# Optimization experiments

Hardware: AMD Instinct MI355X
Metric: run time of the kernel (lower is better)

Reference implementation:

```python
import jax, jax.numpy as jnp
import numpy as np

N_NODES = 100000

def graph_conv(x, src, dst, W_rel, W_root, b, num_nodes):
    # PyG GraphConv: out_i = lin_rel(sum_{j in N(i)} x_j) + lin_root(x_i)
    agg = jax.ops.segment_sum(x[src], dst, num_segments=num_nodes)  # [N, F_in]
    return agg @ W_rel + x @ W_root + b


def setup_inputs() -> dict:
    key = jax.random.key(0)
    ks = jax.random.split(key, 8)
    z = jax.random.normal(ks[0], (N_NODES, 64), dtype=jnp.float32)
    edge_index = jax.random.randint(ks[1], (2, 1600000), 0, N_NODES, dtype=jnp.int64)
    def glorot(k, fi, fo):
        s = (6.0 / (fi + fo)) ** 0.5
        return jax.random.uniform(k, (fi, fo), dtype=jnp.float32, minval=-s, maxval=s)
    return {
        "z": z,
        "edge_index": edge_index,
        "W_rel1": glorot(ks[2], 64, 32), "W_root1": glorot(ks[3], 64, 32), "b1": jnp.zeros((32,), jnp.float32),
        "W_rel2": glorot(ks[4], 32, 16), "W_root2": glorot(ks[5], 32, 16), "b2": jnp.zeros((16,), jnp.float32),
        "W_rel3": glorot(ks[6], 16, 2), "W_root3": glorot(ks[7], 16, 2), "b3": jnp.zeros((2,), jnp.float32),
    }


def reference(z, edge_index, W_rel1, W_root1, b1, W_rel2, W_root2, b2, W_rel3, W_root3, b3):
    src, dst = edge_index[0], edge_index[1]
    h = graph_conv(z, src, dst, W_rel1, W_root1, b1, N_NODES)
    h = jax.nn.relu(h)
    h = graph_conv(h, src, dst, W_rel2, W_root2, b2, N_NODES)
    h = jax.nn.relu(h)
    h = graph_conv(h, src, dst, W_rel3, W_root3, b3, N_NODES)
    return jax.nn.softmax(h, axis=-1)
```

## Files before the change

### kernel.cpp

```cpp
#include <hip/hip_runtime.h>
#include <hip/hip_bf16.h>


#define RNODES 128
#define NB_MAX 1024
#define CH 8192

template <int Fin, int Fout, bool RELU>
__global__ void linear2_kernel(const float* __restrict__ x,
                               const float* __restrict__ Wrel,
                               const float* __restrict__ Wroot,
                               const float* __restrict__ bias,
                               float* __restrict__ t,
                               float* __restrict__ acc, int N) {
    const bool rootTask = (blockIdx.y != 0);
    const float* __restrict__ W = rootTask ? Wroot : Wrel;
    float* __restrict__ outp    = rootTask ? acc : t;

    int n = blockIdx.x * blockDim.x + threadIdx.x;
    if (n >= N) return;

    float o[Fout];
#pragma unroll
    for (int f = 0; f < Fout; ++f) o[f] = 0.f;

    const float* xr = x + (size_t)n * Fin;
    for (int k0 = 0; k0 < Fin; k0 += 16) {
#pragma unroll
        for (int k = 0; k < 16; k += 4) {
            float4 v = *(const float4*)(xr + k0 + k);
            if (RELU) {
                v.x = fmaxf(v.x, 0.f); v.y = fmaxf(v.y, 0.f);
                v.z = fmaxf(v.z, 0.f); v.w = fmaxf(v.w, 0.f);
            }
            const float xv[4] = {v.x, v.y, v.z, v.w};
#pragma unroll
            for (int kk = 0; kk < 4; ++kk) {
                const float* wr = W + (size_t)(k0 + k + kk) * Fout;
#pragma unroll
                for (int f = 0; f < Fout; ++f)
                    o[f] = fmaf(xv[kk], wr[f], o[f]);
            }
        }
    }
    if (rootTask) {
#pragma unroll
        for (int f = 0; f < Fout; ++f) o[f] += bias[f];
    }
    float* op = outp + (size_t)n * Fout;
    if constexpr (Fout >= 4) {
#pragma unroll
        for (int f = 0; f < Fout; f += 4)
            *(float4*)(op + f) = make_float4(o[f], o[f + 1], o[f + 2], o[f + 3]);
    } else {
        *(float2*)op = make_float2(o[0], o[1]);
    }
}

__global__ void hist_coarse_kernel(const int* __restrict__ dst,
                                   int* __restrict__ gcount, int nE, int NB) {
    __shared__ int h[NB_MAX];
    for (int i = threadIdx.x; i < NB; i += blockDim.x) h[i] = 0;
    __syncthreads();
    int stride = gridDim.x * blockDim.x;
    for (int e = blockIdx.x * blockDim.x + threadIdx.x; e < nE; e += stride)
        atomicAdd(&h[dst[e] >> 7], 1);
    __syncthreads();
    for (int i = threadIdx.x; i < NB; i += blockDim.x)
        if (h[i]) atomicAdd(&gcount[i], h[i]);
}

__global__ void scan_buckets_kernel(const int* __restrict__ gcount,
                                    int* __restrict__ bptr,
                                    int* __restrict__ gcursor, int NB, int nE) {
    __shared__ int s[NB_MAX];
    int t = threadIdx.x;
    int own = (t < NB) ? gcount[t] : 0;
    s[t] = own;
    __syncthreads();
    for (int off = 1; off < NB_MAX; off <<= 1) {
        int v = (t >= off) ? s[t - off] : 0;
        __syncthreads();
        s[t] += v;
        __syncthreads();
    }
    if (t < NB) {
        int ex = s[t] - own;
        bptr[t]    = ex;
        gcursor[t] = ex;
    }
    if (t == 0) bptr[NB] = nE;
}

__global__ void bucketize_chunked_kernel(const int* __restrict__ src,
                                         const int* __restrict__ dst,
                                         int* __restrict__ gcursor,
                                         unsigned int* __restrict__ records,
                                         int nE, int NB) {
    __shared__ int chist[NB_MAX];
    __shared__ int sbase[NB_MAX];
    const int e0 = blockIdx.x * CH;
    const int e1 = min(e0 + CH, nE);

    for (int b = threadIdx.x; b < NB; b += blockDim.x) chist[b] = 0;
    __syncthreads();
    for (int e = e0 + threadIdx.x; e < e1; e += blockDim.x)
        atomicAdd(&chist[dst[e] >> 7], 1);
    __syncthreads();
    for (int b = threadIdx.x; b < NB; b += blockDim.x) {
        int c = chist[b];
        sbase[b] = c ? atomicAdd(&gcursor[b], c) : 0;
        chist[b] = 0;
    }
    __syncthreads();
    for (int e = e0 + threadIdx.x; e < e1; e += blockDim.x) {
        int d = dst[e];
        int b = d >> 7;
        int l = atomicAdd(&chist[b], 1);
        records[sbase[b] + l] = (unsigned int)src[e] | ((unsigned int)(d & 127) << 17);
    }
}

__global__ void place_merge_kernel(const unsigned int* __restrict__ records,
                                   const int* __restrict__ bptr,
                                   int* __restrict__ rowptr,
                                   int* __restrict__ srcs_sorted,
                                   int N, int nE, int NB) {
    __shared__ int hist[RNODES];
    __shared__ int s[RNODES];
    __shared__ int lcur[RNODES];
    const int b    = blockIdx.x;
    const int base = b * RNODES;
    const int nn   = min(RNODES, N - base);
    const int beg  = bptr[b], end = bptr[b + 1];
    const int t    = threadIdx.x;

    if (t < RNODES) hist[t] = 0;
    __syncthreads();
    for (int i = beg + t; i < end; i += blockDim.x)
        atomicAdd(&hist[records[i] >> 17], 1);
    __syncthreads();

    if (t < RNODES) s[t] = hist[t];
    __syncthreads();
    for (int off = 1; off < RNODES; off <<= 1) {
        int v = (t < RNODES && t >= off) ? s[t - off] : 0;
        __syncthreads();
        if (t < RNODES && t >= off) s[t] += v;
        __syncthreads();
    }
    if (t < nn) {
        int ex = beg + s[t] - hist[t];
        rowptr[base + t] = ex;
        lcur[t] = ex;
    }
    if (b == NB - 1 && t == 0) rowptr[N] = nE;
    __syncthreads();

    for (int i = beg + t; i < end; i += blockDim.x) {
        unsigned int rec = records[i];
        int pos = atomicAdd(&lcur[rec >> 17], 1);
        srcs_sorted[pos] = (int)(rec & 0x1FFFFu);
    }
}

template <int F, int U, bool SOFTMAX>
__global__ void gather_agg_kernel(const float* __restrict__ t,
                                  const int* __restrict__ rowptr,
                                  const int* __restrict__ srcs,
                                  const float* __restrict__ rootacc,
                                  float* __restrict__ out, int N) {
    int tid = blockIdx.x * blockDim.x + threadIdx.x;
    int n = tid / F;
    if (n >= N) return;
    int f = tid & (F - 1);
    const float* tf = t + f;
    int beg = rowptr[n], end = rowptr[n + 1];
    float sum = 0.0f;
    int e = beg;
    for (; e + U <= end; e += U) {
        int s[U];
        float v[U];
#pragma unroll
        for (int u = 0; u < U; ++u) s[u] = srcs[e + u];
#pragma unroll
        for (int u = 0; u < U; ++u) v[u] = tf[(long)s[u] * F];
#pragma unroll
        for (int u = 0; u < U; ++u) sum += v[u];
    }
    for (; e < end; ++e) sum += tf[(long)srcs[e] * F];

    float v = rootacc[(long)n * F + f] + sum;
    if (!SOFTMAX) {
        out[(long)n * F + f] = v;
    } else {
        float o = __shfl_xor(v, 1, 64);
        float m = fmaxf(v, o);
        float ev = __expf(v - m), eo = __expf(o - m);
        out[(long)n * F + f] = ev / (ev + eo);
    }
}

template <int F>
__global__ void scatter_kernel(const float* __restrict__ t,
                               const int* __restrict__ src,
                               const int* __restrict__ dst,
                               float* __restrict__ acc, int nE) {
    int tid = blockIdx.x * blockDim.x + threadIdx.x;
    int e = tid / F;
    if (e >= nE) return;
    int f = tid & (F - 1);
    atomicAdd(acc + (long)dst[e] * F + f, t[(long)src[e] * F + f]);
}

__global__ void softmax2_kernel(const float* __restrict__ h, float* __restrict__ out, int N) {
    int n = blockIdx.x * blockDim.x + threadIdx.x;
    if (n >= N) return;
    float a = h[2 * n], b = h[2 * n + 1];
    float m = fmaxf(a, b);
    float ea = __expf(a - m), eb = __expf(b - m);
    float inv = 1.0f / (ea + eb);
    out[2 * n] = ea * inv;
    out[2 * n + 1] = eb * inv;
}

extern "C" void kernel_launch(void* const* d_in, const int* in_sizes, int n_in,
                              void* d_out, int out_size, void* d_ws, size_t ws_size,
                              hipStream_t stream) {
    const float* z      = (const float*)d_in[0];
    const int*   ei     = (const int*)d_in[1];
    const float* Wrel1  = (const float*)d_in[2];
    const float* Wroot1 = (const float*)d_in[3];
    const float* b1     = (const float*)d_in[4];
    const float* Wrel2  = (const float*)d_in[5];
    const float* Wroot2 = (const float*)d_in[6];
    const float* b2     = (const float*)d_in[7];
    const float* Wrel3  = (const float*)d_in[8];
    const float* Wroot3 = (const float*)d_in[9];
    const float* b3     = (const float*)d_in[10];

    const int N  = in_sizes[0] / 64;
    const int nE = in_sizes[1] / 2;
    const int* src = ei;
    const int* dst = ei + nE;
    const int NB = (N + RNODES - 1) / RNODES;

    float* regionA = (float*)d_ws;
    float* regionB = regionA + (size_t)N * 32;
    float* t1 = regionA;
    float* h1 = regionB;
    float* t2 = regionA;
    float* h2 = regionA + (size_t)N * 16;
    float* t3 = regionB;
    float* h3 = regionB + (size_t)N * 2;
    unsigned int* records = (unsigned int*)regionA;

    int* ibase       = (int*)(regionB + (size_t)N * 32);
    int* gcount      = ibase;
    int* bptr        = gcount + NB_MAX;
    int* gcursor     = bptr + NB_MAX + 1;
    int* rowptr      = gcursor + NB_MAX;
    int* srcs_sorted = rowptr + N + 1;

    size_t needed = (size_t)N * 64 * sizeof(float)
                  + ((size_t)3 * NB_MAX + 1 + (size_t)N + 1 + (size_t)nE) * sizeof(int);

    const int B = 256;
    const int nodeBlocks  = (N + B - 1) / B;
    const int chunkBlocks = (nE + CH - 1) / CH;
    const dim3 linGrid(nodeBlocks, 2);
    const bool packOK = (N <= (1 << 17)) && (NB <= NB_MAX) && ((size_t)nE * 4 <= (size_t)N * 32 * 4);

    if (ws_size >= needed && packOK) {
        hipMemsetAsync(gcount, 0, (size_t)NB * sizeof(int), stream);
        hist_coarse_kernel<<<256, B, 0, stream>>>(dst, gcount, nE, NB);
        scan_buckets_kernel<<<1, NB_MAX, 0, stream>>>(gcount, bptr, gcursor, NB, nE);
        bucketize_chunked_kernel<<<chunkBlocks, B, 0, stream>>>(src, dst, gcursor, records, nE, NB);
        place_merge_kernel<<<NB, B, 0, stream>>>(records, bptr, rowptr, srcs_sorted, N, nE, NB);

        linear2_kernel<64, 32, false><<<linGrid, B, 0, stream>>>(z, Wrel1, Wroot1, b1, t1, h1, N);
        gather_agg_kernel<32, 8, false><<<((size_t)N * 32 + B - 1) / B, B, 0, stream>>>(
            t1, rowptr, srcs_sorted, h1, h1, N);

        linear2_kernel<32, 16, true><<<linGrid, B, 0, stream>>>(h1, Wrel2, Wroot2, b2, t2, h2, N);
        gather_agg_kernel<16, 8, false><<<((size_t)N * 16 + B - 1) / B, B, 0, stream>>>(
            t2, rowptr, srcs_sorted, h2, h2, N);

        linear2_kernel<16, 2, true><<<linGrid, B, 0, stream>>>(h2, Wrel3, Wroot3, b3, t3, h3, N);
        gather_agg_kernel<2, 4, true><<<((size_t)N * 2 + B - 1) / B, B, 0, stream>>>(
            t3, rowptr, srcs_sorted, h3, (float*)d_out, N);
    } else {
        linear2_kernel<64, 32, false><<<linGrid, B, 0, stream>>>(z, Wrel1, Wroot1, b1, t1, h1, N);
        scatter_kernel<32><<<((size_t)nE * 32 + B - 1) / B, B, 0, stream>>>(t1, src, dst, h1, nE);
        linear2_kernel<32, 16, true><<<linGrid, B, 0, stream>>>(h1, Wrel2, Wroot2, b2, t2, h2, N);
        scatter_kernel<16><<<((size_t)nE * 16 + B - 1) / B, B, 0, stream>>>(t2, src, dst, h2, nE);
        linear2_kernel<16, 2, true><<<linGrid, B, 0, stream>>>(h2, Wrel3, Wroot3, b3, t3, h3, N);
        scatter_kernel<2><<<((size_t)nE * 2 + B - 1) / B, B, 0, stream>>>(t3, src, dst, h3, nE);
        softmax2_kernel<<<nodeBlocks, B, 0, stream>>>(h3, (float*)d_out, N);
    }
}
```

Baseline: 281.7 us.

## Replace atomic bucket cursors with per-chunk histogram prefix scan for bucketing

The edge bucketing now stores a histogram for each chunk, scans it across chunks for every bucket, and gives each chunk a fixed base offset. This removes the second histogram pass inside bucketize and the global atomic cursors, and it also drops the memset. Bucketize no longer builds its own histogram, so dst is read one fewer time. The hist and bucketize kernels now run 1024 threads per block, and one extra kernel launch is added for the per-bucket scan over chunks.

After: 253.0 us. 10.2% less time.

```diff
diff --git a/kernel.cpp b/kernel.cpp
--- a/kernel.cpp
+++ b/kernel.cpp
@@ -5,6 +5,7 @@
 #define RNODES 128
 #define NB_MAX 1024
 #define CH 8192
+#define CMAX 256
 
 template <int Fin, int Fout, bool RELU>
 __global__ void linear2_kernel(const float* __restrict__ x,
@@ -57,25 +58,45 @@
     }
 }
 
-__global__ void hist_coarse_kernel(const int* __restrict__ dst,
-                                   int* __restrict__ gcount, int nE, int NB) {
+__global__ void hist_chunked_kernel(const int* __restrict__ dst,
+                                    int* __restrict__ chunkhist,
+                                    int nE, int NB) {
     __shared__ int h[NB_MAX];
-    for (int i = threadIdx.x; i < NB; i += blockDim.x) h[i] = 0;
-    __syncthreads();
-    int stride = gridDim.x * blockDim.x;
-    for (int e = blockIdx.x * blockDim.x + threadIdx.x; e < nE; e += stride)
+    const int c  = blockIdx.x;
+    const int e0 = c * CH, e1 = min(e0 + CH, nE);
+    for (int b = threadIdx.x; b < NB; b += blockDim.x) h[b] = 0;
+    __syncthreads();
+    for (int e = e0 + threadIdx.x; e < e1; e += blockDim.x)
         atomicAdd(&h[dst[e] >> 7], 1);
     __syncthreads();
-    for (int i = threadIdx.x; i < NB; i += blockDim.x)
-        if (h[i]) atomicAdd(&gcount[i], h[i]);
-}
-
-__global__ void scan_buckets_kernel(const int* __restrict__ gcount,
-                                    int* __restrict__ bptr,
-                                    int* __restrict__ gcursor, int NB, int nE) {
+    for (int b = threadIdx.x; b < NB; b += blockDim.x)
+        chunkhist[(size_t)c * NB + b] = h[b];
+}
+
+__global__ void scan_chunkhist_kernel(int* __restrict__ chunkhist,
+                                      int* __restrict__ gtotal,
+                                      int C, int NB) {
+    __shared__ int s[CMAX];
+    const int b = blockIdx.x;
+    const int t = threadIdx.x;
+    int v = (t < C) ? chunkhist[(size_t)t * NB + b] : 0;
+    s[t] = v;
+    __syncthreads();
+    for (int off = 1; off < CMAX; off <<= 1) {
+        int u = (t >= off) ? s[t - off] : 0;
+        __syncthreads();
+        s[t] += u;
+        __syncthreads();
+    }
+    if (t < C) chunkhist[(size_t)t * NB + b] = s[t] - v;
+    if (t == CMAX - 1) gtotal[b] = s[t];
+}
+
+__global__ void scan_buckets_kernel(const int* __restrict__ gtotal,
+                                    int* __restrict__ bptr, int NB, int nE) {
     __shared__ int s[NB_MAX];
     int t = threadIdx.x;
-    int own = (t < NB) ? gcount[t] : 0;
+    int own = (t < NB) ? gtotal[t] : 0;
     s[t] = own;
     __syncthreads();
     for (int off = 1; off < NB_MAX; off <<= 1) {
@@ -84,40 +105,27 @@
         s[t] += v;
         __syncthreads();
     }
-    if (t < NB) {
-        int ex = s[t] - own;
-        bptr[t]    = ex;
-        gcursor[t] = ex;
-    }
+    if (t < NB) bptr[t] = s[t] - own;
     if (t == 0) bptr[NB] = nE;
 }
 
-__global__ void bucketize_chunked_kernel(const int* __restrict__ src,
-                                         const int* __restrict__ dst,
-                                         int* __restrict__ gcursor,
-                                         unsigned int* __restrict__ records,
-                                         int nE, int NB) {
-    __shared__ int chist[NB_MAX];
-    __shared__ int sbase[NB_MAX];
-    const int e0 = blockIdx.x * CH;
-    const int e1 = min(e0 + CH, nE);
-
-    for (int b = threadIdx.x; b < NB; b += blockDim.x) chist[b] = 0;
-    __syncthreads();
-    for (int e = e0 + threadIdx.x; e < e1; e += blockDim.x)
-        atomicAdd(&chist[dst[e] >> 7], 1);
-    __syncthreads();
-    for (int b = threadIdx.x; b < NB; b += blockDim.x) {
-        int c = chist[b];
-        sbase[b] = c ? atomicAdd(&gcursor[b], c) : 0;
-        chist[b] = 0;
-    }
+__global__ void bucketize_det_kernel(const int* __restrict__ src,
+                                     const int* __restrict__ dst,
+                                     const int* __restrict__ chunkpre,
+                                     const int* __restrict__ bptr,
+                                     unsigned int* __restrict__ records,
+                                     int nE, int NB) {
+    __shared__ int lcur[NB_MAX];
+    const int c  = blockIdx.x;
+    const int e0 = c * CH, e1 = min(e0 + CH, nE);
+    for (int b = threadIdx.x; b < NB; b += blockDim.x)
+        lcur[b] = bptr[b] + chunkpre[(size_t)c * NB + b];
     __syncthreads();
     for (int e = e0 + threadIdx.x; e < e1; e += blockDim.x) {
         int d = dst[e];
         int b = d >> 7;
-        int l = atomicAdd(&chist[b], 1);
-        records[sbase[b] + l] = (unsigned int)src[e] | ((unsigned int)(d & 127) << 17);
+        int pos = atomicAdd(&lcur[b], 1);
+        records[pos] = (unsigned int)src[e] | ((unsigned int)(d & 127) << 17);
     }
 }
 
@@ -244,6 +252,7 @@
     const int* src = ei;
     const int* dst = ei + nE;
     const int NB = (N + RNODES - 1) / RNODES;
+    const int C  = (nE + CH - 1) / CH;
 
     float* regionA = (float*)d_ws;
     float* regionB = regionA + (size_t)N * 32;
@@ -255,27 +264,29 @@
     float* h3 = regionB + (size_t)N * 2;
     unsigned int* records = (unsigned int*)regionA;
 
+    int* chunkhist = (int*)regionB;
+    int* gtotal    = chunkhist + (size_t)CMAX * NB_MAX;
+    int* bptr      = gtotal + NB_MAX;
     int* ibase       = (int*)(regionB + (size_t)N * 32);
-    int* gcount      = ibase;
-    int* bptr        = gcount + NB_MAX;
-    int* gcursor     = bptr + NB_MAX + 1;
-    int* rowptr      = gcursor + NB_MAX;
+    int* rowptr      = ibase;
     int* srcs_sorted = rowptr + N + 1;
 
     size_t needed = (size_t)N * 64 * sizeof(float)
-                  + ((size_t)3 * NB_MAX + 1 + (size_t)N + 1 + (size_t)nE) * sizeof(int);
+                  + ((size_t)N + 1 + (size_t)nE) * sizeof(int);
+    size_t buildNeed = ((size_t)CMAX * NB_MAX + NB_MAX + NB_MAX + 1) * sizeof(int);
 
     const int B = 256;
-    const int nodeBlocks  = (N + B - 1) / B;
-    const int chunkBlocks = (nE + CH - 1) / CH;
+    const int nodeBlocks = (N + B - 1) / B;
     const dim3 linGrid(nodeBlocks, 2);
-    const bool packOK = (N <= (1 << 17)) && (NB <= NB_MAX) && ((size_t)nE * 4 <= (size_t)N * 32 * 4);
+    const bool packOK = (N <= (1 << 17)) && (NB <= NB_MAX) && (C <= CMAX)
+                      && ((size_t)nE * 4 <= (size_t)N * 32 * 4)
+                      && (buildNeed <= (size_t)N * 32 * 4);
 
     if (ws_size >= needed && packOK) {
-        hipMemsetAsync(gcount, 0, (size_t)NB * sizeof(int), stream);
-        hist_coarse_kernel<<<256, B, 0, stream>>>(dst, gcount, nE, NB);
-        scan_buckets_kernel<<<1, NB_MAX, 0, stream>>>(gcount, bptr, gcursor, NB, nE);
-        bucketize_chunked_kernel<<<chunkBlocks, B, 0, stream>>>(src, dst, gcursor, records, nE, NB);
+        hist_chunked_kernel<<<C, 1024, 0, stream>>>(dst, chunkhist, nE, NB);
+        scan_chunkhist_kernel<<<NB, CMAX, 0, stream>>>(chunkhist, gtotal, C, NB);
+        scan_buckets_kernel<<<1, NB_MAX, 0, stream>>>(gtotal, bptr, NB, nE);
+        bucketize_det_kernel<<<C, 1024, 0, stream>>>(src, dst, chunkhist, bptr, records, nE, NB);
         place_merge_kernel<<<NB, B, 0, stream>>>(records, bptr, rowptr, srcs_sorted, N, nE, NB);
 
         linear2_kernel<64, 32, false><<<linGrid, B, 0, stream>>>(z, Wrel1, Wroot1, b1, t1, h1, N);
```
